# Performance work log

Hardware: AMD Instinct MI355X
Metric: run time of the kernel (lower is better)

Reference implementation:

```python
import jax, jax.numpy as jnp
import numpy as np

N = 100000
E = 1600000
C_IN = 128
C_OUT = 128
EPS = 1e-5


def setup_inputs() -> dict:
    key = jax.random.key(0)
    ks = jax.random.split(key, 8)
    x = jax.random.normal(ks[0], (N, C_IN), dtype=jnp.float32)
    edge_index = jax.random.randint(ks[1], (2, E), 0, N, dtype=jnp.int64)
    s_proj = 1.0 / np.sqrt(C_IN)
    s_out = 1.0 / np.sqrt(C_IN)
    W_proj = jax.random.uniform(ks[2], (C_IN, C_IN), jnp.float32, -s_proj, s_proj)
    b_proj = jax.random.uniform(ks[3], (C_IN,), jnp.float32, -s_proj, s_proj)
    W_l = jax.random.uniform(ks[4], (C_OUT, C_IN), jnp.float32, -s_out, s_out)
    b_l = jax.random.uniform(ks[5], (C_OUT,), jnp.float32, -s_out, s_out)
    W_r = jax.random.uniform(ks[6], (C_OUT, C_IN), jnp.float32, -s_out, s_out)
    gamma = jnp.ones((C_OUT,), jnp.float32)
    beta = jnp.zeros((C_OUT,), jnp.float32)
    return {"x": x, "edge_index": edge_index, "W_proj": W_proj, "b_proj": b_proj,
            "W_l": W_l, "b_l": b_l, "W_r": W_r, "gamma": gamma, "beta": beta}


def reference(x, edge_index, W_proj, b_proj, W_l, b_l, W_r, gamma, beta):
    # SAGEConv(project=True, aggr='sum'): project+ReLU source features per node,
    # gather along edges, scatter-sum at targets, then lin_l(agg) + lin_r(x_root).
    src, dst = edge_index[0], edge_index[1]
    h = jax.nn.relu(x @ W_proj.T + b_proj)            # [N, C_IN]
    msg = h[src]                                       # [E, C_IN] edge gather
    agg = jax.ops.segment_sum(msg, dst, num_segments=N)  # [N, C_IN]
    out = agg @ W_l.T + b_l + x @ W_r.T                # [N, C_OUT] (root uses unprojected x)
    # LayerNorm(c_out)
    mu = jnp.mean(out, axis=-1, keepdims=True)
    var = jnp.var(out, axis=-1, keepdims=True)
    return (out - mu) * jax.lax.rsqrt(var + EPS) * gamma + beta
```

## Files before the change

### kernel.cpp

```cpp
#include <hip/hip_runtime.h>
#include <stdint.h>

#define NN 100000
#define NE 1600000
#define C  128
#define NB 782
#define CAP 4096
#define SB_SHIFT 13
#define MB 782
#define P1B 250
#define MBO 782

typedef __attribute__((ext_vector_type(8))) short short8;
typedef __attribute__((ext_vector_type(4))) float f32x4;

__device__ __forceinline__ float bf2f(uint16_t u) {
  union { uint32_t u; float f; } v; v.u = ((uint32_t)u) << 16; return v.f;
}
__device__ __forceinline__ uint16_t f2bf(float f) {
  union { float f; uint32_t u; } v; v.f = f;
  uint32_t r = v.u + 0x7fffu + ((v.u >> 16) & 1u);
  return (uint16_t)(r >> 16);
}
__device__ __forceinline__ float2 bf2x2(uint32_t u) {
  return make_float2(bf2f((uint16_t)u), bf2f((uint16_t)(u >> 16)));
}
__device__ __forceinline__ short8 cvt_row8(const float* p) {
  float4 u = *(const float4*)p;
  float4 v = *(const float4*)(p + 4);
  short8 av;
  av[0] = (short)f2bf(u.x); av[1] = (short)f2bf(u.y);
  av[2] = (short)f2bf(u.z); av[3] = (short)f2bf(u.w);
  av[4] = (short)f2bf(v.x); av[5] = (short)f2bf(v.y);
  av[6] = (short)f2bf(v.z); av[7] = (short)f2bf(v.w);
  return av;
}

__global__ __launch_bounds__(256) void cast3_k(
    const float* __restrict__ a, const float* __restrict__ b, const float* __restrict__ c,
    uint16_t* __restrict__ oa, uint16_t* __restrict__ ob, uint16_t* __restrict__ oc)
{
  int i = blockIdx.x * 256 + threadIdx.x;
  int which = i >> 12, j = i & 4095;
  const float* s = which == 0 ? a : (which == 1 ? b : c);
  uint16_t* d    = which == 0 ? oa : (which == 1 ? ob : oc);
  float4 v = ((const float4*)s)[j];
  uint2 p;
  p.x = (uint32_t)f2bf(v.x) | ((uint32_t)f2bf(v.y) << 16);
  p.y = (uint32_t)f2bf(v.z) | ((uint32_t)f2bf(v.w) << 16);
  ((uint2*)d)[j] = p;
}


__global__ __launch_bounds__(512) void fused_front_k(
    const float* __restrict__ x, const uint16_t* __restrict__ wpb,
    const float* __restrict__ bp, uint16_t* __restrict__ h,
    const int* __restrict__ esrc, const int* __restrict__ edst,
    int* __restrict__ gcnt, uint32_t* __restrict__ ebuf)
{
  extern __shared__ uint8_t slds[];
  const int t = threadIdx.x;

  if (blockIdx.x < MB) {
#pragma unroll
    for (int qq = 0; qq < 4; ++qq) {
      int ci = qq * 512 + t;
      int cl = ci >> 4, k16 = ci & 15;
      *(short8*)(slds + cl * 256 + ((k16 ^ (cl & 15)) << 4)) =
          *(const short8*)(wpb + ci * 8);
    }
    __syncthreads();

    const int w = t >> 6, lane = t & 63;
    const int tile_m0 = blockIdx.x * 128;
    const int r16 = lane & 15, g = lane >> 4;
    const int row = tile_m0 + w * 16 + r16;
    const int arow = row < NN ? row : NN - 1;

    short8 a[4];
    const float* xp = x + (size_t)arow * C + g * 8;
#pragma unroll
    for (int kk = 0; kk < 4; ++kk) a[kk] = cvt_row8(xp + kk * 32);

    f32x4 hp[8];
#pragma unroll
    for (int nt = 0; nt < 8; ++nt) {
      f32x4 p = {0.f, 0.f, 0.f, 0.f};
      const int cidx = nt * 16 + r16;
      const uint8_t* rbp = slds + cidx * 256;
#pragma unroll
      for (int kk = 0; kk < 4; ++kk) {
        int slot = (((kk << 2) + g) ^ (cidx & 15)) << 4;
        p = __builtin_amdgcn_mfma_f32_16x16x32_bf16(*(const short8*)(rbp + slot), a[kk], p, 0, 0, 0);
      }
      hp[nt] = p;
    }
    __syncthreads();

    const int lrow = w * 16 + r16;
#pragma unroll
    for (int nt = 0; nt < 8; ++nt) {
      const int col0 = nt * 16 + g * 4;
      float4 bp4 = *(const float4*)(bp + col0);
      float h0 = hp[nt][0] + bp4.x, h1 = hp[nt][1] + bp4.y;
      float h2 = hp[nt][2] + bp4.z, h3 = hp[nt][3] + bp4.w;
      h0 = h0 > 0.f ? h0 : 0.f; h1 = h1 > 0.f ? h1 : 0.f;
      h2 = h2 > 0.f ? h2 : 0.f; h3 = h3 > 0.f ? h3 : 0.f;
      uint2 ph;
      ph.x = (uint32_t)f2bf(h0) | ((uint32_t)f2bf(h1) << 16);
      ph.y = (uint32_t)f2bf(h2) | ((uint32_t)f2bf(h3) << 16);
      *(uint2*)(slds + lrow * 256 + ((col0 * 2) ^ ((lrow & 15) << 4))) = ph;
    }
    __syncthreads();

#pragma unroll
    for (int i = 0; i < 4; ++i) {
      const int ofs = i * 8192 + t * 16;
      const int trow = ofs >> 8;
      const int inrow = ofs & 255;
      const int grow = tile_m0 + trow;
      if (grow < NN)
        *(uint4*)(h + (size_t)grow * C + (inrow >> 1)) =
            *(const uint4*)(slds + (trow << 8) + (inrow ^ ((trow & 15) << 4)));
    }
  } else {
    int* bh = (int*)slds;
    int* gb = bh + NB;
    const int blk = blockIdx.x - MB;
    const int base = blk * 6400;

    for (int i = t; i < NB; i += 512) bh[i] = 0;

    const int4* ed4 = (const int4*)(edst + base);
    const int4* es4 = (const int4*)(esrc + base);
    int4 dv[4], sv[4];
    bool val[4];
#pragma unroll
    for (int k = 0; k < 4; ++k) {
      int i = t + k * 512;
      val[k] = (i < 1600);
      if (val[k]) { dv[k] = ed4[i]; sv[k] = es4[i]; }
    }
    __syncthreads();

#pragma unroll
    for (int k = 0; k < 4; ++k) if (val[k]) {
      atomicAdd(&bh[dv[k].x >> 7], 1); atomicAdd(&bh[dv[k].y >> 7], 1);
      atomicAdd(&bh[dv[k].z >> 7], 1); atomicAdd(&bh[dv[k].w >> 7], 1);
    }
    __syncthreads();

    for (int i = t; i < NB; i += 512) {
      int c = bh[i];
      gb[i] = c ? atomicAdd(&gcnt[i], c) : 0;
      bh[i] = 0;
    }
    __syncthreads();

#define P1_SCATTER(d, s) do { \
      int bb = (d) >> 7; \
      int o = atomicAdd(&bh[bb], 1); \
      int pos = gb[bb] + o; \
      if (pos < CAP) ebuf[(size_t)bb * CAP + pos] = ((uint32_t)((d) & 127) << 17) | (uint32_t)(s); \
    } while (0)

#pragma unroll
    for (int k = 0; k < 4; ++k) if (val[k]) {
      P1_SCATTER(dv[k].x, sv[k].x); P1_SCATTER(dv[k].y, sv[k].y);
      P1_SCATTER(dv[k].z, sv[k].z); P1_SCATTER(dv[k].w, sv[k].w);
    }
#undef P1_SCATTER
  }
}

__global__ __launch_bounds__(256) void phase2_k(
    const uint32_t* __restrict__ ebuf, const int* __restrict__ gcnt,
    int* __restrict__ ssrc, int2* __restrict__ sdeg)
{
  __shared__ uint32_t raw[CAP];
  __shared__ int lout[CAP];
  __shared__ int cnt2[128 * 16];
  __shared__ int nd[128];
  __shared__ int psum[256];
  const int b = blockIdx.x, t = threadIdx.x;
  const int n0 = b * 128;

  int acc = 0;
  for (int i = t; i < b; i += 256) acc += gcnt[i];
  psum[t] = acc;
  __syncthreads();
  for (int off = 128; off > 0; off >>= 1) {
    if (t < off) psum[t] += psum[t + off];
    __syncthreads();
  }
  const int base = psum[0];
  int cnt = gcnt[b]; if (cnt > CAP) cnt = CAP;

  for (int i = t; i < 128 * 16; i += 256) cnt2[i] = 0;
  __syncthreads();
  for (int i = t; i < cnt; i += 256) {
    uint32_t v = ebuf[(size_t)b * CAP + i];
    raw[i] = v;
    atomicAdd(&cnt2[(v >> 17) * 16 + ((v & 0x1FFFFu) >> SB_SHIFT)], 1);
  }
  __syncthreads();

  int deg_t = 0;
  if (t < 128) {
#pragma unroll
    for (int i = 0; i < 16; ++i) deg_t += cnt2[t * 16 + i];
    nd[t] = deg_t;
  }
  __syncthreads();
  for (int off = 1; off < 128; off <<= 1) {
    int v = 0;
    if (t < 128 && t >= off) v = nd[t - off];
    __syncthreads();
    if (t < 128) nd[t] += v;
    __syncthreads();
  }
  if (t < 128) {
    int pref = nd[t] - deg_t;
    if (n0 + t < NN) sdeg[n0 + t] = make_int2(base + pref, deg_t);
    int run = pref;
#pragma unroll
    for (int i = 0; i < 16; ++i) { int c = cnt2[t * 16 + i]; cnt2[t * 16 + i] = run; run += c; }
  }
  __syncthreads();
  for (int i = t; i < cnt; i += 256) {
    uint32_t v = raw[i];
    int o = atomicAdd(&cnt2[(v >> 17) * 16 + ((v & 0x1FFFFu) >> SB_SHIFT)], 1);
    lout[o] = (int)(v & 0x1FFFFu);
  }
  __syncthreads();
  for (int i = t; i < cnt; i += 256) ssrc[base + i] = lout[i];
}

__global__ __launch_bounds__(256) void aggregate_k(
    const uint16_t* __restrict__ h, const int* __restrict__ ssrc,
    const int2* __restrict__ sdeg, uint16_t* __restrict__ agg)
{
  const int wid = (blockIdx.x * 256 + threadIdx.x) >> 6;
  if (wid >= NN) return;
  const int lane = threadIdx.x & 63;
  const int q = lane >> 4;
  const int l16 = lane & 15;
  const int2 sd = sdeg[wid];
  const int s0 = sd.x, cnt = sd.y;
  const size_t choff = (size_t)l16 * 8;
  float2 a0 = {0.f, 0.f}, a1 = {0.f, 0.f}, a2 = {0.f, 0.f}, a3 = {0.f, 0.f};

#define ACC8(v) do { \
    a0 += bf2x2((v).x); a1 += bf2x2((v).y); \
    a2 += bf2x2((v).z); a3 += bf2x2((v).w); \
  } while (0)

  int j = 0;
  if (cnt >= 16) {
    int e0 = ssrc[s0 + q];
    int e1 = ssrc[s0 + 4 + q];
    int e2 = ssrc[s0 + 8 + q];
    int e3 = ssrc[s0 + 12 + q];
    for (; j + 16 <= cnt;) {
      uint4 v0 = *(const uint4*)(h + (size_t)e0 * C + choff);
      uint4 v1 = *(const uint4*)(h + (size_t)e1 * C + choff);
      uint4 v2 = *(const uint4*)(h + (size_t)e2 * C + choff);
      uint4 v3 = *(const uint4*)(h + (size_t)e3 * C + choff);
      j += 16;
      if (j + 16 <= cnt) {
        e0 = ssrc[s0 + j + q];
        e1 = ssrc[s0 + j + 4 + q];
        e2 = ssrc[s0 + j + 8 + q];
        e3 = ssrc[s0 + j + 12 + q];
      }
      ACC8(v0); ACC8(v1); ACC8(v2); ACC8(v3);
    }
  }
  const int rem = cnt - j;
  if (rem > 0) {
    int i0 = j + ((q      < rem) ? q      : 0);
    int i1 = j + ((q + 4  < rem) ? q + 4  : 0);
    int i2 = j + ((q + 8  < rem) ? q + 8  : 0);
    int i3 = j + ((q + 12 < rem) ? q + 12 : 0);
    int e0 = ssrc[s0 + i0];
    int e1 = ssrc[s0 + i1];
    int e2 = ssrc[s0 + i2];
    int e3 = ssrc[s0 + i3];
    uint4 v0 = *(const uint4*)(h + (size_t)e0 * C + choff);
    uint4 v1 = *(const uint4*)(h + (size_t)e1 * C + choff);
    uint4 v2 = *(const uint4*)(h + (size_t)e2 * C + choff);
    uint4 v3 = *(const uint4*)(h + (size_t)e3 * C + choff);
    if (q < rem)      ACC8(v0);
    if (q + 4 < rem)  ACC8(v1);
    if (q + 8 < rem)  ACC8(v2);
    if (q + 12 < rem) ACC8(v3);
  }
#undef ACC8

#pragma unroll
  for (int msk = 16; msk <= 32; msk <<= 1) {
    a0.x += __shfl_xor(a0.x, msk, 64); a0.y += __shfl_xor(a0.y, msk, 64);
    a1.x += __shfl_xor(a1.x, msk, 64); a1.y += __shfl_xor(a1.y, msk, 64);
    a2.x += __shfl_xor(a2.x, msk, 64); a2.y += __shfl_xor(a2.y, msk, 64);
    a3.x += __shfl_xor(a3.x, msk, 64); a3.y += __shfl_xor(a3.y, msk, 64);
  }
  if (q == 0) {
    uint4 p;
    p.x = (uint32_t)f2bf(a0.x) | ((uint32_t)f2bf(a0.y) << 16);
    p.y = (uint32_t)f2bf(a1.x) | ((uint32_t)f2bf(a1.y) << 16);
    p.z = (uint32_t)f2bf(a2.x) | ((uint32_t)f2bf(a2.y) << 16);
    p.w = (uint32_t)f2bf(a3.x) | ((uint32_t)f2bf(a3.y) << 16);
    *(uint4*)(agg + (size_t)wid * C + choff) = p;
  }
}

__global__ __launch_bounds__(512) void gemm_out_k(
    const uint16_t* __restrict__ aggb, const float* __restrict__ x,
    const uint16_t* __restrict__ wlb, const uint16_t* __restrict__ wrb,
    const float* __restrict__ bl, const float* __restrict__ gamma,
    const float* __restrict__ beta, float* __restrict__ out)
{
  extern __shared__ uint8_t slds[];
  const int t = threadIdx.x;
#pragma unroll
  for (int qq = 0; qq < 8; ++qq) {
    int ci = qq * 512 + t;
    int m  = ci >> 11;
    int cj = ci & 2047;
    int cl = cj >> 4, k16 = cj & 15;
    const uint16_t* wsrc = m == 0 ? wlb : wrb;
    *(short8*)(slds + m * 32768 + cl * 256 + ((k16 ^ (cl & 15)) << 4)) =
        *(const short8*)(wsrc + cj * 8);
  }
  __syncthreads();

  const int w = t >> 6, lane = t & 63;
  const int tile_m = blockIdx.x * 128 + w * 16;
  if (tile_m >= NN) return;
  const int r16 = lane & 15, g = lane >> 4;

  const int row = tile_m + r16;
  const int arow = row < NN ? row : NN - 1;
  short8 a0[4], a1[4];
  const uint16_t* p0 = aggb + (size_t)arow * C + g * 8;
  const float* xp = x + (size_t)arow * C + g * 8;
#pragma unroll
  for (int kk = 0; kk < 4; ++kk) {
    a0[kk] = *(const short8*)(p0 + kk * 32);
    a1[kk] = cvt_row8(xp + kk * 32);
  }

  f32x4 acc[8];
  float s1 = 0.f, s2 = 0.f;
#pragma unroll
  for (int nt = 0; nt < 8; ++nt) {
    f32x4 c4 = {0.f, 0.f, 0.f, 0.f};
    const int c = nt * 16 + r16;
    const uint8_t* rbl = slds + c * 256;
    const uint8_t* rbr = slds + 32768 + c * 256;
#pragma unroll
    for (int kk = 0; kk < 4; ++kk) {
      int slot = (((kk << 2) + g) ^ (c & 15)) << 4;
      c4 = __builtin_amdgcn_mfma_f32_16x16x32_bf16(*(const short8*)(rbl + slot), a0[kk], c4, 0, 0, 0);
      c4 = __builtin_amdgcn_mfma_f32_16x16x32_bf16(*(const short8*)(rbr + slot), a1[kk], c4, 0, 0, 0);
    }
    const int col0 = nt * 16 + g * 4;
    float4 bl4 = *(const float4*)(bl + col0);
    c4[0] += bl4.x; c4[1] += bl4.y; c4[2] += bl4.z; c4[3] += bl4.w;
#pragma unroll
    for (int rr = 0; rr < 4; ++rr) { s1 += c4[rr]; s2 += c4[rr] * c4[rr]; }
    acc[nt] = c4;
  }

  s1 += __shfl_xor(s1, 16, 64); s2 += __shfl_xor(s2, 16, 64);
  s1 += __shfl_xor(s1, 32, 64); s2 += __shfl_xor(s2, 32, 64);
  const float mean = s1 * (1.f / C);
  const float var = s2 * (1.f / C) - mean * mean;
  const float rstd = rsqrtf(var + 1e-5f);

  if (row < NN) {
#pragma unroll
    for (int nt = 0; nt < 8; ++nt) {
      const int col0 = nt * 16 + g * 4;
      float4 gm = *(const float4*)(gamma + col0);
      float4 bt = *(const float4*)(beta + col0);
      float4 o;
      o.x = (acc[nt][0] - mean) * rstd * gm.x + bt.x;
      o.y = (acc[nt][1] - mean) * rstd * gm.y + bt.y;
      o.z = (acc[nt][2] - mean) * rstd * gm.z + bt.z;
      o.w = (acc[nt][3] - mean) * rstd * gm.w + bt.w;
      *(float4*)(out + (size_t)row * C + col0) = o;
    }
  }
}

extern "C" void kernel_launch(void* const* d_in, const int* in_sizes, int n_in,
                              void* d_out, int out_size, void* d_ws, size_t ws_size,
                              hipStream_t stream)
{
  const float* x        = (const float*)d_in[0];
  const int* ei         = (const int*)d_in[1];
  const float* Wp       = (const float*)d_in[2];
  const float* bp       = (const float*)d_in[3];
  const float* Wl       = (const float*)d_in[4];
  const float* bl       = (const float*)d_in[5];
  const float* Wr       = (const float*)d_in[6];
  const float* gamma    = (const float*)d_in[7];
  const float* beta     = (const float*)d_in[8];
  float* out            = (float*)d_out;

  char* ws = (char*)d_ws;
  uint16_t* h    = (uint16_t*)(ws + 0);
  uint32_t* ebuf = (uint32_t*)(ws + 25600000);
  uint16_t* aggb = (uint16_t*)(ws + 25600000);
  uint16_t* wpb  = (uint16_t*)(ws + 76800000);
  uint16_t* wlb  = (uint16_t*)(ws + 76832768);
  uint16_t* wrb  = (uint16_t*)(ws + 76865536);
  int2* sdeg     = (int2*)(ws + 76898304);
  int* gcnt      = (int*)(ws + 77698304);
  int* ssrc      = (int*)(ws + 78102400);

  const int* esrc = ei;
  const int* edst = ei + NE;

  hipMemsetAsync(gcnt, 0, NB * sizeof(int), stream);

  cast3_k<<<48, 256, 0, stream>>>(Wp, Wl, Wr, wpb, wlb, wrb);

  fused_front_k<<<MB + P1B, 512, 32768, stream>>>(
      x, wpb, bp, h, esrc, edst, gcnt, ebuf);

  phase2_k<<<NB, 256, 0, stream>>>(ebuf, gcnt, ssrc, sdeg);

  aggregate_k<<<(NN + 3) / 4, 256, 0, stream>>>(h, ssrc, sdeg, aggb);

  gemm_out_k<<<MBO, 512, 65536, stream>>>(aggb, x, wlb, wrb, bl, gamma, beta, out);
}
```

Measured before the change: 144.2 us.

## Fuse edge bucketing and neighbor aggregation into one kernel using LDS-resident edge lists

Merges the phase2 sort kernel and the aggregate kernel into a single 1024-thread kernel per 128-node bucket. The sorted source indices stay in shared memory (lout) and are read by the aggregation loop, so the global ssrc/sdeg arrays, the prefix sum over bucket counts and one launch all go away. In exchange, only 782 blocks of 1024 threads do the gather, which lowers the parallelism and occupancy available to hide the latency of the irregular h-row loads. The prefetch of the next indices is also dropped, and the aggregation cannot start until the sort inside the block finishes.

```diff
diff --git a/kernel.cpp b/kernel.cpp
--- a/kernel.cpp
+++ b/kernel.cpp
@@ -173,32 +173,22 @@
   }
 }
 
-__global__ __launch_bounds__(256) void phase2_k(
+__global__ __launch_bounds__(1024) void p2agg_k(
     const uint32_t* __restrict__ ebuf, const int* __restrict__ gcnt,
-    int* __restrict__ ssrc, int2* __restrict__ sdeg)
+    const uint16_t* __restrict__ h, uint16_t* __restrict__ agg)
 {
   __shared__ uint32_t raw[CAP];
   __shared__ int lout[CAP];
   __shared__ int cnt2[128 * 16];
   __shared__ int nd[128];
-  __shared__ int psum[256];
+  __shared__ int sstart[128];
+  __shared__ int sdegl[128];
   const int b = blockIdx.x, t = threadIdx.x;
-  const int n0 = b * 128;
-
-  int acc = 0;
-  for (int i = t; i < b; i += 256) acc += gcnt[i];
-  psum[t] = acc;
-  __syncthreads();
-  for (int off = 128; off > 0; off >>= 1) {
-    if (t < off) psum[t] += psum[t + off];
-    __syncthreads();
-  }
-  const int base = psum[0];
   int cnt = gcnt[b]; if (cnt > CAP) cnt = CAP;
 
-  for (int i = t; i < 128 * 16; i += 256) cnt2[i] = 0;
-  __syncthreads();
-  for (int i = t; i < cnt; i += 256) {
+  for (int i = t; i < 128 * 16; i += 1024) cnt2[i] = 0;
+  __syncthreads();
+  for (int i = t; i < cnt; i += 1024) {
     uint32_t v = ebuf[(size_t)b * CAP + i];
     raw[i] = v;
     atomicAdd(&cnt2[(v >> 17) * 16 + ((v & 0x1FFFFu) >> SB_SHIFT)], 1);
@@ -221,97 +211,86 @@
   }
   if (t < 128) {
     int pref = nd[t] - deg_t;
-    if (n0 + t < NN) sdeg[n0 + t] = make_int2(base + pref, deg_t);
+    sstart[t] = pref; sdegl[t] = deg_t;
     int run = pref;
 #pragma unroll
     for (int i = 0; i < 16; ++i) { int c = cnt2[t * 16 + i]; cnt2[t * 16 + i] = run; run += c; }
   }
   __syncthreads();
-  for (int i = t; i < cnt; i += 256) {
+  for (int i = t; i < cnt; i += 1024) {
     uint32_t v = raw[i];
     int o = atomicAdd(&cnt2[(v >> 17) * 16 + ((v & 0x1FFFFu) >> SB_SHIFT)], 1);
     lout[o] = (int)(v & 0x1FFFFu);
   }
   __syncthreads();
-  for (int i = t; i < cnt; i += 256) ssrc[base + i] = lout[i];
-}
-
-__global__ __launch_bounds__(256) void aggregate_k(
-    const uint16_t* __restrict__ h, const int* __restrict__ ssrc,
-    const int2* __restrict__ sdeg, uint16_t* __restrict__ agg)
-{
-  const int wid = (blockIdx.x * 256 + threadIdx.x) >> 6;
-  if (wid >= NN) return;
-  const int lane = threadIdx.x & 63;
+
+  const int w = t >> 6, lane = t & 63;
   const int q = lane >> 4;
   const int l16 = lane & 15;
-  const int2 sd = sdeg[wid];
-  const int s0 = sd.x, cnt = sd.y;
   const size_t choff = (size_t)l16 * 8;
-  float2 a0 = {0.f, 0.f}, a1 = {0.f, 0.f}, a2 = {0.f, 0.f}, a3 = {0.f, 0.f};
 
 #define ACC8(v) do { \
     a0 += bf2x2((v).x); a1 += bf2x2((v).y); \
     a2 += bf2x2((v).z); a3 += bf2x2((v).w); \
   } while (0)
 
-  int j = 0;
-  if (cnt >= 16) {
-    int e0 = ssrc[s0 + q];
-    int e1 = ssrc[s0 + 4 + q];
-    int e2 = ssrc[s0 + 8 + q];
-    int e3 = ssrc[s0 + 12 + q];
-    for (; j + 16 <= cnt;) {
+#pragma unroll 1
+  for (int ni = 0; ni < 8; ++ni) {
+    const int nl = w + ni * 16;
+    const int node = b * 128 + nl;
+    const int s0 = sstart[nl];
+    const int cn = sdegl[nl];
+    float2 a0 = {0.f, 0.f}, a1 = {0.f, 0.f}, a2 = {0.f, 0.f}, a3 = {0.f, 0.f};
+
+    int j = 0;
+    for (; j + 16 <= cn; j += 16) {
+      int e0 = lout[s0 + j + q];
+      int e1 = lout[s0 + j + 4 + q];
+      int e2 = lout[s0 + j + 8 + q];
+      int e3 = lout[s0 + j + 12 + q];
       uint4 v0 = *(const uint4*)(h + (size_t)e0 * C + choff);
       uint4 v1 = *(const uint4*)(h + (size_t)e1 * C + choff);
       uint4 v2 = *(const uint4*)(h + (size_t)e2 * C + choff);
       uint4 v3 = *(const uint4*)(h + (size_t)e3 * C + choff);
-      j += 16;
-      if (j + 16 <= cnt) {
-        e0 = ssrc[s0 + j + q];
-        e1 = ssrc[s0 + j + 4 + q];
-        e2 = ssrc[s0 + j + 8 + q];
-        e3 = ssrc[s0 + j + 12 + q];
-      }
       ACC8(v0); ACC8(v1); ACC8(v2); ACC8(v3);
     }
-  }
-  const int rem = cnt - j;
-  if (rem > 0) {
-    int i0 = j + ((q      < rem) ? q      : 0);
-    int i1 = j + ((q + 4  < rem) ? q + 4  : 0);
-    int i2 = j + ((q + 8  < rem) ? q + 8  : 0);
-    int i3 = j + ((q + 12 < rem) ? q + 12 : 0);
-    int e0 = ssrc[s0 + i0];
-    int e1 = ssrc[s0 + i1];
-    int e2 = ssrc[s0 + i2];
-    int e3 = ssrc[s0 + i3];
-    uint4 v0 = *(const uint4*)(h + (size_t)e0 * C + choff);
-    uint4 v1 = *(const uint4*)(h + (size_t)e1 * C + choff);
-    uint4 v2 = *(const uint4*)(h + (size_t)e2 * C + choff);
-    uint4 v3 = *(const uint4*)(h + (size_t)e3 * C + choff);
-    if (q < rem)      ACC8(v0);
-    if (q + 4 < rem)  ACC8(v1);
-    if (q + 8 < rem)  ACC8(v2);
-    if (q + 12 < rem) ACC8(v3);
+    const int rem = cn - j;
+    if (rem > 0) {
+      int i0 = j + ((q      < rem) ? q      : 0);
+      int i1 = j + ((q + 4  < rem) ? q + 4  : 0);
+      int i2 = j + ((q + 8  < rem) ? q + 8  : 0);
+      int i3 = j + ((q + 12 < rem) ? q + 12 : 0);
+      int e0 = lout[s0 + i0];
+      int e1 = lout[s0 + i1];
+      int e2 = lout[s0 + i2];
+      int e3 = lout[s0 + i3];
+      uint4 v0 = *(const uint4*)(h + (size_t)e0 * C + choff);
+      uint4 v1 = *(const uint4*)(h + (size_t)e1 * C + choff);
+      uint4 v2 = *(const uint4*)(h + (size_t)e2 * C + choff);
+      uint4 v3 = *(const uint4*)(h + (size_t)e3 * C + choff);
+      if (q < rem)      ACC8(v0);
+      if (q + 4 < rem)  ACC8(v1);
+      if (q + 8 < rem)  ACC8(v2);
+      if (q + 12 < rem) ACC8(v3);
+    }
+
+#pragma unroll
+    for (int msk = 16; msk <= 32; msk <<= 1) {
+      a0.x += __shfl_xor(a0.x, msk, 64); a0.y += __shfl_xor(a0.y, msk, 64);
+      a1.x += __shfl_xor(a1.x, msk, 64); a1.y += __shfl_xor(a1.y, msk, 64);
+      a2.x += __shfl_xor(a2.x, msk, 64); a2.y += __shfl_xor(a2.y, msk, 64);
+      a3.x += __shfl_xor(a3.x, msk, 64); a3.y += __shfl_xor(a3.y, msk, 64);
+    }
+    if (q == 0 && node < NN) {
+      uint4 p;
+      p.x = (uint32_t)f2bf(a0.x) | ((uint32_t)f2bf(a0.y) << 16);
+      p.y = (uint32_t)f2bf(a1.x) | ((uint32_t)f2bf(a1.y) << 16);
+      p.z = (uint32_t)f2bf(a2.x) | ((uint32_t)f2bf(a2.y) << 16);
+      p.w = (uint32_t)f2bf(a3.x) | ((uint32_t)f2bf(a3.y) << 16);
+      *(uint4*)(agg + (size_t)node * C + choff) = p;
+    }
   }
 #undef ACC8
-
-#pragma unroll
-  for (int msk = 16; msk <= 32; msk <<= 1) {
-    a0.x += __shfl_xor(a0.x, msk, 64); a0.y += __shfl_xor(a0.y, msk, 64);
-    a1.x += __shfl_xor(a1.x, msk, 64); a1.y += __shfl_xor(a1.y, msk, 64);
-    a2.x += __shfl_xor(a2.x, msk, 64); a2.y += __shfl_xor(a2.y, msk, 64);
-    a3.x += __shfl_xor(a3.x, msk, 64); a3.y += __shfl_xor(a3.y, msk, 64);
-  }
-  if (q == 0) {
-    uint4 p;
-    p.x = (uint32_t)f2bf(a0.x) | ((uint32_t)f2bf(a0.y) << 16);
-    p.y = (uint32_t)f2bf(a1.x) | ((uint32_t)f2bf(a1.y) << 16);
-    p.z = (uint32_t)f2bf(a2.x) | ((uint32_t)f2bf(a2.y) << 16);
-    p.w = (uint32_t)f2bf(a3.x) | ((uint32_t)f2bf(a3.y) << 16);
-    *(uint4*)(agg + (size_t)wid * C + choff) = p;
-  }
 }
 
 __global__ __launch_bounds__(512) void gemm_out_k(
@@ -412,13 +391,11 @@
   char* ws = (char*)d_ws;
   uint16_t* h    = (uint16_t*)(ws + 0);
   uint32_t* ebuf = (uint32_t*)(ws + 25600000);
-  uint16_t* aggb = (uint16_t*)(ws + 25600000);
-  uint16_t* wpb  = (uint16_t*)(ws + 76800000);
-  uint16_t* wlb  = (uint16_t*)(ws + 76832768);
-  uint16_t* wrb  = (uint16_t*)(ws + 76865536);
-  int2* sdeg     = (int2*)(ws + 76898304);
-  int* gcnt      = (int*)(ws + 77698304);
-  int* ssrc      = (int*)(ws + 78102400);
+  uint16_t* aggb = (uint16_t*)(ws + 38412288);
+  uint16_t* wpb  = (uint16_t*)(ws + 64012288);
+  uint16_t* wlb  = (uint16_t*)(ws + 64045056);
+  uint16_t* wrb  = (uint16_t*)(ws + 64077824);
+  int* gcnt      = (int*)(ws + 64110592);
 
   const int* esrc = ei;
   const int* edst = ei + NE;
@@ -430,9 +407,7 @@
   fused_front_k<<<MB + P1B, 512, 32768, stream>>>(
       x, wpb, bp, h, esrc, edst, gcnt, ebuf);
 
-  phase2_k<<<NB, 256, 0, stream>>>(ebuf, gcnt, ssrc, sdeg);
-
-  aggregate_k<<<(NN + 3) / 4, 256, 0, stream>>>(h, ssrc, sdeg, aggb);
+  p2agg_k<<<NB, 1024, 0, stream>>>(ebuf, gcnt, h, aggb);
 
   gemm_out_k<<<MBO, 512, 65536, stream>>>(aggb, x, wlb, wrb, bl, gamma, beta, out);
 }
```

New measurement: 138.1 us. 1.04x faster.
